# Kernel optimization log

Measured on AMD Instinct MI355X. Metric: run time of the kernel, lower is better.

The kernel has to match this reference:

```python
import jax, jax.numpy as jnp
import numpy as np

B, N, L, M = 256, 1024, 128, 512


def setup_inputs() -> dict:
    key = jax.random.key(0)
    k1, k2 = jax.random.split(key)
    patches = jax.random.normal(k1, (B, N, L), dtype=jnp.float32)
    masked_indices = jax.random.randint(k2, (B, M), 0, N, dtype=jnp.int64)
    return {"patches": patches, "masked_indices": masked_indices}


def reference(patches, masked_indices):
    # For each (b, idx in masked_indices[b]): replace patches[b, idx] with
    # linspace(patches[b, idx, 0], patches[b, idx, -1], steps=L).
    b_, n_, l_ = patches.shape
    brow = jnp.arange(b_)[:, None]                       # [B,1] batch index broadcast
    start = patches[brow, masked_indices, 0]             # [B,M]
    end = patches[brow, masked_indices, l_ - 1]          # [B,M]
    # torch.linspace: start + t*(end-start), t = i/(L-1)
    t = (jnp.arange(l_, dtype=patches.dtype) / (l_ - 1))  # [L]
    new_patches = start[..., None] + (end - start)[..., None] * t  # [B,M,L]
    out = patches.at[brow, masked_indices].set(new_patches)
    return out
```

## Files before the change

### kernel.cpp

```cpp
#include <hip/hip_runtime.h>

constexpr int B = 256;
constexpr int N = 1024;
constexpr int L = 128;
constexpr int M = 512;

__global__ void flag_kernel(const int* __restrict__ idx,
                            unsigned char* __restrict__ flags) {
    int i = blockIdx.x * blockDim.x + threadIdx.x;
    if (i < B * M) {
        int b = i >> 9;
        int n = idx[i];
        flags[b * N + n] = 1;
    }
}

__global__ void main_kernel(const float* __restrict__ in,
                            const unsigned char* __restrict__ flags,
                            float* __restrict__ out) {
    int t = blockIdx.x * blockDim.x + threadIdx.x;
    int row  = t >> 5;
    int quad = t & 31;
    const float* rowp = in + (size_t)row * L;
    float* outp = out + (size_t)row * L + quad * 4;

    if (flags[row]) {
        float s = rowp[0];
        float e = rowp[L - 1];
        float d = e - s;
        int l0 = quad * 4;
        float4 v;
        v.x = s + d * ((float)(l0 + 0) * (1.0f / 127.0f));
        v.y = s + d * ((float)(l0 + 1) * (1.0f / 127.0f));
        v.z = s + d * ((float)(l0 + 2) * (1.0f / 127.0f));
        v.w = s + d * ((float)(l0 + 3) * (1.0f / 127.0f));
        *(float4*)outp = v;
    } else {
        *(float4*)outp = *(const float4*)(rowp + quad * 4);
    }
}

extern "C" void kernel_launch(void* const* d_in, const int* in_sizes, int n_in,
                              void* d_out, int out_size, void* d_ws, size_t ws_size,
                              hipStream_t stream) {
    const float* patches = (const float*)d_in[0];
    const int* masked    = (const int*)d_in[1];
    float* out           = (float*)d_out;
    unsigned char* flags = (unsigned char*)d_ws;

    hipMemsetAsync(flags, 0, (size_t)B * N, stream);

    {
        int total = B * M;
        int block = 256;
        int grid = (total + block - 1) / block;
        flag_kernel<<<grid, block, 0, stream>>>(masked, flags);
    }
    {
        long long total = (long long)B * N * 32;
        int block = 256;
        long long grid = (total + block - 1) / block;
        main_kernel<<<(int)grid, block, 0, stream>>>(patches, flags, out);
    }
}
```

Baseline: 228.9 us.

## Fuse flag building into main kernel using per-block shared-memory flags

Replaces the memset, the flag-scatter kernel and the copy/interpolate kernel with one kernel. Each block owns a quarter of a batch row and rebuilds that batch's mask flags in shared memory from the index list, then grid-strides over its slice of rows. This removes two extra launches and the global flag round trip. In exchange each batch's indices are read SPLIT times, and the grid is only 1024 blocks with per-thread loops, which may lower memory-level parallelism on this large copy.

```diff
diff --git a/kernel.cpp b/kernel.cpp
--- a/kernel.cpp
+++ b/kernel.cpp
@@ -4,39 +4,47 @@
 constexpr int N = 1024;
 constexpr int L = 128;
 constexpr int M = 512;
+constexpr int SPLIT = 4;
+constexpr int BLOCK = 256;
 
-__global__ void flag_kernel(const int* __restrict__ idx,
-                            unsigned char* __restrict__ flags) {
-    int i = blockIdx.x * blockDim.x + threadIdx.x;
-    if (i < B * M) {
-        int b = i >> 9;
-        int n = idx[i];
-        flags[b * N + n] = 1;
-    }
-}
+__global__ __launch_bounds__(BLOCK) void fused_kernel(
+        const float* __restrict__ in,
+        const int* __restrict__ idx,
+        float* __restrict__ out) {
+    const int b    = blockIdx.x / SPLIT;
+    const int part = blockIdx.x % SPLIT;
 
-__global__ void main_kernel(const float* __restrict__ in,
-                            const unsigned char* __restrict__ flags,
-                            float* __restrict__ out) {
-    int t = blockIdx.x * blockDim.x + threadIdx.x;
-    int row  = t >> 5;
-    int quad = t & 31;
-    const float* rowp = in + (size_t)row * L;
-    float* outp = out + (size_t)row * L + quad * 4;
+    __shared__ unsigned char flags[N];
+    for (int i = threadIdx.x; i < N; i += BLOCK) flags[i] = 0;
+    __syncthreads();
+    for (int i = threadIdx.x; i < M; i += BLOCK) flags[idx[b * M + i]] = 1;
+    __syncthreads();
 
-    if (flags[row]) {
-        float s = rowp[0];
-        float e = rowp[L - 1];
-        float d = e - s;
-        int l0 = quad * 4;
+    const float* bin  = in  + (size_t)b * (N * L);
+    float*       bout = out + (size_t)b * (N * L);
+
+    constexpr int QUADS_PER_BATCH = N * L / 4;
+    constexpr int QUADS_PER_PART  = QUADS_PER_BATCH / SPLIT;
+    const int base = part * QUADS_PER_PART;
+
+    for (int i = threadIdx.x; i < QUADS_PER_PART; i += BLOCK) {
+        const int q    = base + i;
+        const int row  = q >> 5;
+        const int quad = q & 31;
+        const float* rowp = bin + row * L;
         float4 v;
-        v.x = s + d * ((float)(l0 + 0) * (1.0f / 127.0f));
-        v.y = s + d * ((float)(l0 + 1) * (1.0f / 127.0f));
-        v.z = s + d * ((float)(l0 + 2) * (1.0f / 127.0f));
-        v.w = s + d * ((float)(l0 + 3) * (1.0f / 127.0f));
-        *(float4*)outp = v;
-    } else {
-        *(float4*)outp = *(const float4*)(rowp + quad * 4);
+        if (flags[row]) {
+            const float s = rowp[0];
+            const float d = rowp[L - 1] - s;
+            const int l0 = quad * 4;
+            v.x = fmaf(d, (float)(l0 + 0) * (1.0f / 127.0f), s);
+            v.y = fmaf(d, (float)(l0 + 1) * (1.0f / 127.0f), s);
+            v.z = fmaf(d, (float)(l0 + 2) * (1.0f / 127.0f), s);
+            v.w = fmaf(d, (float)(l0 + 3) * (1.0f / 127.0f), s);
+        } else {
+            v = ((const float4*)bin)[q];
+        }
+        ((float4*)bout)[q] = v;
     }
 }
 
@@ -46,20 +54,6 @@
     const float* patches = (const float*)d_in[0];
     const int* masked    = (const int*)d_in[1];
     float* out           = (float*)d_out;
-    unsigned char* flags = (unsigned char*)d_ws;
 
-    hipMemsetAsync(flags, 0, (size_t)B * N, stream);
-
-    {
-        int total = B * M;
-        int block = 256;
-        int grid = (total + block - 1) / block;
-        flag_kernel<<<grid, block, 0, stream>>>(masked, flags);
-    }
-    {
-        long long total = (long long)B * N * 32;
-        int block = 256;
-        long long grid = (total + block - 1) / block;
-        main_kernel<<<(int)grid, block, 0, stream>>>(patches, flags, out);
-    }
+    fused_kernel<<<B * SPLIT, BLOCK, 0, stream>>>(patches, masked, out);
 }
```

Result: slower. 236.4 us (+3.3%).
